# Kernel tuning notes

Measured on AMD Instinct MI355X. Metric: run time of the kernel, lower is better.

## Reference

```python
import jax, jax.numpy as jnp
import numpy as np

N, H, E, K, C, M = 4096, 512, 512, 64, 128, 4  # tokens, hidden, embed, categories, children/cat, max_num_children
IN = E + H  # LSTMCell input size


def setup_inputs() -> dict:
    key = jax.random.key(0)
    ks = jax.random.split(key, 12)
    s = 0.05
    return {
        "et": jax.random.normal(ks[0], (N, H), jnp.float32),
        "x": jax.random.normal(ks[1], (N, IN), jnp.float32),
        "h": jax.random.normal(ks[2], (N, H), jnp.float32),
        "c": jax.random.normal(ks[3], (N, H), jnp.float32),
        "cat": jax.random.randint(ks[4], (N,), 0, K, jnp.int32),
        "ci": jax.random.randint(ks[5], (N,), 0, M, jnp.int32),
        # per-category prediction Linear(hidden_size -> |children(category)|)
        "W_lin": jax.random.normal(ks[6], (K, C, H), jnp.float32) * s,
        "b_lin": jax.random.normal(ks[7], (K, C), jnp.float32) * s,
        # per-child-index LSTMCell(embedding+hidden -> hidden), torch gate order i,f,g,o
        "W_ih": jax.random.normal(ks[8], (M, 4 * H, IN), jnp.float32) * s,
        "W_hh": jax.random.normal(ks[9], (M, 4 * H, H), jnp.float32) * s,
        "b_ih": jax.random.normal(ks[10], (M, 4 * H), jnp.float32) * s,
        "b_hh": jax.random.normal(ks[11], (M, 4 * H), jnp.float32) * s,
    }


def reference(et, x, h, c, cat, ci, W_lin, b_lin, W_ih, W_hh, b_ih, b_hh):
    # get_log_odds: route each token to its category's Linear (gather weights, per-token matvec)
    Wg = W_lin[cat]                                   # [N, C, H]
    log_odds = jnp.einsum('nh,nch->nc', et, Wg) + b_lin[cat]  # [N, C]

    # get_next: LSTMCell selected by child_index. Only M=4 cells, so compute all
    # cells' gates densely (efficient GEMMs) and select with a one-hot mix.
    gates_all = (jnp.einsum('ni,kgi->nkg', x, W_ih)
                 + jnp.einsum('nh,kgh->nkg', h, W_hh)
                 + (b_ih + b_hh)[None])               # [N, M, 4H]
    sel = jax.nn.one_hot(ci, M, dtype=gates_all.dtype)  # [N, M]
    gates = jnp.einsum('nkg,nk->ng', gates_all, sel)     # [N, 4H]
    i_, f_, g_, o_ = jnp.split(gates, 4, axis=-1)
    c2 = jax.nn.sigmoid(f_) * c + jax.nn.sigmoid(i_) * jnp.tanh(g_)
    h2 = jax.nn.sigmoid(o_) * jnp.tanh(c2)
    return log_odds, h2, c2
```

## Files before the change

kernel.cpp:

```cpp
#include <hip/hip_runtime.h>
#include <hip/hip_bf16.h>
#include <stdint.h>

#define NTOK 4096
#define HID  512
#define INSZ 1024
#define KIN  1536
#define KCAT 64
#define CCH  128
#define MCELL 4
#define G4H  2048
#define SLOTS 4608

typedef unsigned short u16;
typedef __bf16 bf16x8 __attribute__((ext_vector_type(8)));
typedef float  f32x4  __attribute__((ext_vector_type(4)));

__device__ __forceinline__ u16 f2bf(float f) {
    unsigned u = __float_as_uint(f);
    u += 0x7fffu + ((u >> 16) & 1u);
    return (u16)(u >> 16);
}
__device__ __forceinline__ float bf2f(u16 v) {
    return __uint_as_float(((unsigned)v) << 16);
}
__device__ __forceinline__ void store_bf8(u16* p, float4 a, float4 b) {
    ushort4 r0, r1;
    r0.x = f2bf(a.x); r0.y = f2bf(a.y); r0.z = f2bf(a.z); r0.w = f2bf(a.w);
    r1.x = f2bf(b.x); r1.y = f2bf(b.y); r1.z = f2bf(b.z); r1.w = f2bf(b.w);
    *reinterpret_cast<ushort4*>(p) = r0;
    *reinterpret_cast<ushort4*>(p + 4) = r1;
}
__device__ __forceinline__ void gl16(const u16* g, u16* l) {
    __builtin_amdgcn_global_load_lds((const __attribute__((address_space(1))) void*)g,
                                     (__attribute__((address_space(3))) void*)l, 16, 0, 0);
}

#define CH_W  (8192 * 192)
#define CH_L  (8192 * 64)
#define CH_A  (4097 * 192)
#define CH_TOT (CH_W + CH_L + CH_A)
#define PK_BLOCKS 2048

__global__ __launch_bounds__(256) void fat_pack(
    const float* __restrict__ x, const float* __restrict__ h,
    const float* __restrict__ Wih, const float* __restrict__ Whh,
    const float* __restrict__ W_lin,
    const int* __restrict__ ci, const int* __restrict__ cat,
    int* __restrict__ meta, int* __restrict__ perm_ci, int* __restrict__ perm_cat,
    u16* __restrict__ A_tok, u16* __restrict__ Wb, u16* __restrict__ Wlin)
{
    if (blockIdx.x == 0) {
        __shared__ int cnt_ci[MCELL], cur_ci[MCELL];
        __shared__ int cnt_cat[KCAT], cur_cat[KCAT];
        int tid = threadIdx.x;
        if (tid < MCELL) cnt_ci[tid] = 0;
        if (tid < KCAT)  cnt_cat[tid] = 0;
        __syncthreads();
        for (int t = tid; t < NTOK; t += 256) {
            atomicAdd(&cnt_ci[ci[t]], 1);
            atomicAdd(&cnt_cat[cat[t]], 1);
        }
        __syncthreads();
        if (tid == 0) {
            int off = 0;
            for (int m = 0; m < MCELL; ++m) {
                int p = (cnt_ci[m] + 127) & ~127;
                meta[m] = p; meta[4 + m] = off; cur_ci[m] = off; off += p;
            }
            off = 0;
            for (int i = 0; i < 128; ++i) meta[136 + i] = -1;
            for (int k = 0; k < KCAT; ++k) {
                int p = (cnt_cat[k] + 63) & ~63;
                meta[8 + k] = p; meta[72 + k] = off; cur_cat[k] = off;
                for (int i = 0; i < p / 64; ++i) meta[136 + off / 64 + i] = k;
                off += p;
            }
        }
        __syncthreads();
        for (int i = tid; i < SLOTS; i += 256) perm_ci[i] = -1;
        for (int i = tid; i < 8192; i += 256) perm_cat[i] = -1;
        __syncthreads();
        for (int t = tid; t < NTOK; t += 256) {
            perm_ci[atomicAdd(&cur_ci[ci[t]], 1)] = t;
            perm_cat[atomicAdd(&cur_cat[cat[t]], 1)] = t;
        }
        return;
    }
    for (int i = (blockIdx.x - 1) * 256 + threadIdx.x; i < CH_TOT; i += (PK_BLOCKS - 1) * 256) {
        if (i < CH_W) {
            int row = i / 192, cc = i - row * 192;
            int m = row >> 11, j = row & 2047;
            int srow = (j & 3) * HID + (j >> 2);
            int c = cc * 8;
            const float* src = (c < INSZ) ? (Wih + ((size_t)m * G4H + srow) * INSZ + c)
                                          : (Whh + ((size_t)m * G4H + srow) * HID + (c - INSZ));
            store_bf8(Wb + (size_t)row * KIN + c,
                      *(const float4*)src, *(const float4*)(src + 4));
        } else if (i < CH_W + CH_L) {
            int i2 = i - CH_W;
            int row = i2 >> 6, cc = i2 & 63;
            const float* src = W_lin + (size_t)row * HID + cc * 8;
            store_bf8(Wlin + (size_t)row * HID + cc * 8,
                      *(const float4*)src, *(const float4*)(src + 4));
        } else {
            int i3 = i - (CH_W + CH_L);
            int row = i3 / 192, cc = i3 - row * 192;
            int c = cc * 8;
            u16* dst = A_tok + (size_t)row * KIN + c;
            if (row == NTOK) {
                *reinterpret_cast<int4*>(dst) = make_int4(0, 0, 0, 0);
            } else {
                const float* src = (c < INSZ) ? (x + (size_t)row * INSZ + c)
                                              : (h + (size_t)row * HID + (c - INSZ));
                store_bf8(dst, *(const float4*)src, *(const float4*)(src + 4));
            }
        }
    }
}

#define FENCE() __builtin_amdgcn_sched_barrier(0)

__global__ __launch_bounds__(256, 2) void mega_gemm(
    const u16* __restrict__ A_tok,
    const u16* __restrict__ Wb,
    const u16* __restrict__ Wlin,
    const float* __restrict__ et,
    const float* __restrict__ b_lin,
    const float* __restrict__ c,
    const float* __restrict__ b_ih,
    const float* __restrict__ b_hh,
    const int* __restrict__ meta,
    const int* __restrict__ perm_ci,
    const int* __restrict__ perm_cat,
    float* __restrict__ out)
{
    __shared__ __align__(16) u16 S[32768];
    __shared__ int sperm[128];

    int tid = threadIdx.x;
    int lane = tid & 63, wave = tid >> 6;
    int qd = lane >> 4, l15 = lane & 15;
    int rsw = l15 & 7;

    int id = blockIdx.x;
    if (id < 2048) {
        int g = id & 63;
        int rt = id >> 6;
        int m = g >> 4, ct = g & 15;
        int pcnt = meta[m];
        if (rt * 128 >= pcnt) return;
        int row0 = meta[4 + m] + rt * 128;

        if (tid < 128) sperm[tid] = perm_ci[row0 + tid];
        __syncthreads();

        const u16* gA[4]; const u16* gB[4];
        int qq[4];
        #pragma unroll
        for (int j = 0; j < 4; ++j) {
            int q = j * 256 + tid;
            int row = q >> 3, kc = (q & 7) ^ (row & 7);
            int t = sperm[row];
            gA[j] = A_tok + (size_t)(t >= 0 ? t : NTOK) * KIN + kc * 8;
            gB[j] = Wb + ((size_t)m * G4H + ct * 128 + row) * KIN + kc * 8;
            qq[j] = q * 8;
        }

        int wm = wave >> 1, wn = wave & 1;

        f32x4 acc[4][4];
        #pragma unroll
        for (int i = 0; i < 4; ++i)
            #pragma unroll
            for (int j = 0; j < 4; ++j)
                acc[i][j] = (f32x4){0.f, 0.f, 0.f, 0.f};

#define STAGE(ABASE, BBASE) do { \
        _Pragma("unroll") \
        for (int j = 0; j < 4; ++j) { gl16(gA[j], &S[(ABASE) + qq[j]]); gA[j] += 64; } \
        _Pragma("unroll") \
        for (int j = 0; j < 4; ++j) { gl16(gB[j], &S[(BBASE) + qq[j]]); gB[j] += 64; } \
    } while (0)

#define GEMM_STEP(ABASE, BBASE) do { \
        _Pragma("unroll") \
        for (int ks2 = 0; ks2 < 2; ++ks2) { \
            int ch = (ks2 * 4 + qd) ^ rsw; \
            bf16x8 fb[4]; \
            _Pragma("unroll") \
            for (int tj = 0; tj < 4; ++tj) \
                fb[tj] = *reinterpret_cast<const bf16x8*>(&S[(BBASE) + (wn * 64 + tj * 16 + l15) * 64 + ch * 8]); \
            _Pragma("unroll") \
            for (int ti = 0; ti < 4; ++ti) { \
                bf16x8 fa = *reinterpret_cast<const bf16x8*>(&S[(ABASE) + (wm * 64 + ti * 16 + l15) * 64 + ch * 8]); \
                _Pragma("unroll") \
                for (int tj = 0; tj < 4; ++tj) \
                    acc[ti][tj] = __builtin_amdgcn_mfma_f32_16x16x32_bf16(fa, fb[tj], acc[ti][tj], 0, 0, 0); \
            } \
        } \
    } while (0)

        STAGE(0, 16384);
        for (int ks = 0; ks < 24; ks += 2) {
            STAGE(8192, 24576);
            asm volatile("s_waitcnt vmcnt(8)" ::: "memory");
            FENCE();
            __builtin_amdgcn_s_barrier();
            FENCE();
            GEMM_STEP(0, 16384);
            FENCE();
            __builtin_amdgcn_s_barrier();
            FENCE();
            if (ks + 2 < 24) {
                STAGE(0, 16384);
                asm volatile("s_waitcnt vmcnt(8)" ::: "memory");
            } else {
                asm volatile("s_waitcnt vmcnt(0)" ::: "memory");
            }
            FENCE();
            __builtin_amdgcn_s_barrier();
            FENCE();
            GEMM_STEP(8192, 24576);
            FENCE();
            __builtin_amdgcn_s_barrier();
            FENCE();
        }
#undef STAGE
#undef GEMM_STEP

        int gt = l15 & 3;
        float bias[4];
        #pragma unroll
        for (int tj = 0; tj < 4; ++tj) {
            int u = ct * 32 + wn * 16 + tj * 4 + (l15 >> 2);
            bias[tj] = b_ih[m * G4H + gt * HID + u] + b_hh[m * G4H + gt * HID + u];
        }
        int b0 = lane & 1, b1 = lane & 2;
        const size_t o_h2 = (size_t)NTOK * CCH;
        const size_t o_c2 = o_h2 + (size_t)NTOK * HID;
        #pragma unroll
        for (int ti = 0; ti < 4; ++ti) {
            int t = sperm[wm * 64 + ti * 16 + qd * 4 + (lane & 3)];
            #pragma unroll
            for (int tj = 0; tj < 4; ++tj) {
                float v0 = acc[ti][tj][0] + bias[tj];
                float v1 = acc[ti][tj][1] + bias[tj];
                float v2 = acc[ti][tj][2] + bias[tj];
                float v3 = acc[ti][tj][3] + bias[tj];
                float tmp;
                tmp = __shfl_xor(b0 ? v0 : v1, 1); if (b0) v0 = tmp; else v1 = tmp;
                tmp = __shfl_xor(b0 ? v2 : v3, 1); if (b0) v2 = tmp; else v3 = tmp;
                tmp = __shfl_xor(b1 ? v0 : v2, 2); if (b1) v0 = tmp; else v2 = tmp;
                tmp = __shfl_xor(b1 ? v1 : v3, 2); if (b1) v1 = tmp; else v3 = tmp;
                if (t >= 0) {
                    int u = ct * 32 + wn * 16 + tj * 4 + (l15 >> 2);
                    float si = 1.f / (1.f + __expf(-v0));
                    float sf = 1.f / (1.f + __expf(-v1));
                    float tg = tanhf(v2);
                    float so = 1.f / (1.f + __expf(-v3));
                    float cold = c[(size_t)t * HID + u];
                    float c2 = sf * cold + si * tg;
                    float h2 = so * tanhf(c2);
                    out[o_h2 + (size_t)t * HID + u] = h2;
                    out[o_c2 + (size_t)t * HID + u] = c2;
                }
            }
        }
    } else {
        u16* As = S;
        u16* Bs = S + 8192;
        int rtl = id - 2048;
        int k = meta[136 + rtl];
        if (k < 0) return;
        int r0 = rtl * 64;

        if (tid < 64) sperm[tid] = perm_cat[r0 + tid];
        __syncthreads();

        int rb = tid >> 3;
        int kc = (tid & 7) ^ (rb & 7);

        const u16* gW[4]; u16* lW[4];
        #pragma unroll
        for (int i = 0; i < 4; ++i) {
            gW[i] = Wlin + ((size_t)k * CCH + i * 32 + rb) * HID + kc * 8;
            lW[i] = As + (i * 256 + wave * 64) * 8;
        }
        int ar = tid >> 2;
        int acp = tid & 3;
        int at = sperm[ar];
        const float* asrc = (at >= 0) ? (et + (size_t)at * HID) : nullptr;

        f32x4 acc[4][2];
        #pragma unroll
        for (int i = 0; i < 4; ++i) {
            acc[i][0] = (f32x4){0.f, 0.f, 0.f, 0.f};
            acc[i][1] = (f32x4){0.f, 0.f, 0.f, 0.f};
        }

        for (int kk = 0; kk < HID; kk += 64) {
            #pragma unroll
            for (int i = 0; i < 4; ++i) { gl16(gW[i], lW[i]); gW[i] += 64; }
            #pragma unroll
            for (int j = 0; j < 2; ++j) {
                int dch = acp * 2 + j;
                int sch = dch ^ (ar & 7);
                u16* dst = &Bs[ar * 64 + dch * 8];
                if (asrc) {
                    const float* s = asrc + kk + sch * 8;
                    store_bf8(dst, *(const float4*)s, *(const float4*)(s + 4));
                } else {
                    *reinterpret_cast<int4*>(dst) = make_int4(0, 0, 0, 0);
                }
            }
            __syncthreads();
            #pragma unroll
            for (int ks2 = 0; ks2 < 2; ++ks2) {
                int ch = (ks2 * 4 + qd) ^ rsw;
                bf16x8 fa[4], fb[2];
                #pragma unroll
                for (int ti = 0; ti < 4; ++ti)
                    fa[ti] = *reinterpret_cast<const bf16x8*>(&Bs[(ti * 16 + l15) * 64 + ch * 8]);
                #pragma unroll
                for (int tj = 0; tj < 2; ++tj)
                    fb[tj] = *reinterpret_cast<const bf16x8*>(&As[(wave * 32 + tj * 16 + l15) * 64 + ch * 8]);
                #pragma unroll
                for (int ti = 0; ti < 4; ++ti)
                    #pragma unroll
                    for (int tj = 0; tj < 2; ++tj)
                        acc[ti][tj] = __builtin_amdgcn_mfma_f32_16x16x32_bf16(fa[ti], fb[tj], acc[ti][tj], 0, 0, 0);
            }
            __syncthreads();
        }

        #pragma unroll
        for (int ti = 0; ti < 4; ++ti) {
            #pragma unroll
            for (int tj = 0; tj < 2; ++tj) {
                int n = wave * 32 + tj * 16 + l15;
                float bias = b_lin[k * CCH + n];
                #pragma unroll
                for (int rr = 0; rr < 4; ++rr) {
                    int row = ti * 16 + qd * 4 + rr;
                    int t = sperm[row];
                    if (t >= 0)
                        out[(size_t)t * CCH + n] = acc[ti][tj][rr] + bias;
                }
            }
        }
    }
}

extern "C" void kernel_launch(void* const* d_in, const int* in_sizes, int n_in,
                              void* d_out, int out_size, void* d_ws, size_t ws_size,
                              hipStream_t stream) {
    const float* et    = (const float*)d_in[0];
    const float* x     = (const float*)d_in[1];
    const float* h     = (const float*)d_in[2];
    const float* c     = (const float*)d_in[3];
    const int*   cat   = (const int*)d_in[4];
    const int*   ci    = (const int*)d_in[5];
    const float* W_lin = (const float*)d_in[6];
    const float* b_lin = (const float*)d_in[7];
    const float* W_ih  = (const float*)d_in[8];
    const float* W_hh  = (const float*)d_in[9];
    const float* b_ih  = (const float*)d_in[10];
    const float* b_hh  = (const float*)d_in[11];
    float* out = (float*)d_out;

    char* ws = (char*)d_ws;
    int* meta     = (int*)ws;
    int* perm_ci  = (int*)(ws + 2048);
    int* perm_cat = (int*)(ws + 22528);
    u16* A_tok    = (u16*)(ws + 55296);
    u16* Wb       = (u16*)(ws + 12641280);
    u16* Wlin     = (u16*)(ws + 37807104);

    fat_pack<<<PK_BLOCKS, 256, 0, stream>>>(x, h, W_ih, W_hh, W_lin, ci, cat,
                                            meta, perm_ci, perm_cat, A_tok, Wb, Wlin);

    mega_gemm<<<2048 + 128, 256, 0, stream>>>(A_tok, Wb, Wlin, et, b_lin, c,
                                              b_ih, b_hh, meta, perm_ci, perm_cat, out);
}
```

Measured before the change: 232.1 us.

## Enlarge LSTM GEMM tiles to 256x256 with 512 threads and triple-buffered K=32 pipeline

The LSTM gate GEMM moves from 128x128 tiles with 256 threads to 256x256 tiles with 512 threads (8 waves, 8x4 MFMA accumulators each). It also switches to a three-slab LDS ring with K=32 stages and raises MFMA wave priority. Per-cell padding grows to 256 rows and the category offsets are computed with a parallel prefix scan instead of a serial loop. The category Linear blocks now pack two 64-row tiles per 512-thread block. The larger tiles aim to cut global/LDS traffic per MFMA, at the cost of more padding waste, higher register pressure and fewer blocks.

```diff
diff --git a/kernel.cpp b/kernel.cpp
--- a/kernel.cpp
+++ b/kernel.cpp
@@ -10,7 +10,7 @@
 #define CCH  128
 #define MCELL 4
 #define G4H  2048
-#define SLOTS 4608
+#define SLOTS 5120
 
 typedef unsigned short u16;
 typedef __bf16 bf16x8 __attribute__((ext_vector_type(8)));
@@ -53,6 +53,7 @@
     if (blockIdx.x == 0) {
         __shared__ int cnt_ci[MCELL], cur_ci[MCELL];
         __shared__ int cnt_cat[KCAT], cur_cat[KCAT];
+        __shared__ int scan_cat[KCAT];
         int tid = threadIdx.x;
         if (tid < MCELL) cnt_ci[tid] = 0;
         if (tid < KCAT)  cnt_cat[tid] = 0;
@@ -62,20 +63,27 @@
             atomicAdd(&cnt_cat[cat[t]], 1);
         }
         __syncthreads();
-        if (tid == 0) {
+        for (int i = tid; i < 128; i += 256) meta[136 + i] = -1;
+        if (tid < MCELL) {
             int off = 0;
-            for (int m = 0; m < MCELL; ++m) {
-                int p = (cnt_ci[m] + 127) & ~127;
-                meta[m] = p; meta[4 + m] = off; cur_ci[m] = off; off += p;
-            }
-            off = 0;
-            for (int i = 0; i < 128; ++i) meta[136 + i] = -1;
-            for (int k = 0; k < KCAT; ++k) {
-                int p = (cnt_cat[k] + 63) & ~63;
-                meta[8 + k] = p; meta[72 + k] = off; cur_cat[k] = off;
-                for (int i = 0; i < p / 64; ++i) meta[136 + off / 64 + i] = k;
-                off += p;
-            }
+            for (int i = 0; i < tid; ++i) off += (cnt_ci[i] + 255) & ~255;
+            int p = (cnt_ci[tid] + 255) & ~255;
+            meta[tid] = p; meta[4 + tid] = off; cur_ci[tid] = off;
+        }
+        if (tid < KCAT) scan_cat[tid] = (cnt_cat[tid] + 63) & ~63;
+        __syncthreads();
+        for (int d = 1; d < KCAT; d <<= 1) {
+            int v = 0;
+            if (tid < KCAT && tid >= d) v = scan_cat[tid - d];
+            __syncthreads();
+            if (tid < KCAT) scan_cat[tid] += v;
+            __syncthreads();
+        }
+        if (tid < KCAT) {
+            int p = (cnt_cat[tid] + 63) & ~63;
+            int off = scan_cat[tid] - p;
+            meta[8 + tid] = p; meta[72 + tid] = off; cur_cat[tid] = off;
+            for (int i = 0; i < p / 64; ++i) meta[136 + off / 64 + i] = tid;
         }
         __syncthreads();
         for (int i = tid; i < SLOTS; i += 256) perm_ci[i] = -1;
@@ -120,8 +128,9 @@
 }
 
 #define FENCE() __builtin_amdgcn_sched_barrier(0)
-
-__global__ __launch_bounds__(256, 2) void mega_gemm(
+#define SLAB 16384
+
+__global__ __launch_bounds__(512, 2) void mega_gemm(
     const u16* __restrict__ A_tok,
     const u16* __restrict__ Wb,
     const u16* __restrict__ Wlin,
@@ -135,113 +144,117 @@
     const int* __restrict__ perm_cat,
     float* __restrict__ out)
 {
-    __shared__ __align__(16) u16 S[32768];
-    __shared__ int sperm[128];
+    __shared__ __align__(16) u16 S[3 * SLAB];
+    __shared__ int sperm[256];
 
     int tid = threadIdx.x;
-    int lane = tid & 63, wave = tid >> 6;
+    int lane = tid & 63;
     int qd = lane >> 4, l15 = lane & 15;
-    int rsw = l15 & 7;
 
     int id = blockIdx.x;
-    if (id < 2048) {
-        int g = id & 63;
-        int rt = id >> 6;
-        int m = g >> 4, ct = g & 15;
+    if (id < 512) {
+        int g = id & 31, rt = id >> 5;
+        int m = g >> 3, ct = g & 7;
         int pcnt = meta[m];
-        if (rt * 128 >= pcnt) return;
-        int row0 = meta[4 + m] + rt * 128;
-
-        if (tid < 128) sperm[tid] = perm_ci[row0 + tid];
-        __syncthreads();
-
-        const u16* gA[4]; const u16* gB[4];
-        int qq[4];
-        #pragma unroll
-        for (int j = 0; j < 4; ++j) {
-            int q = j * 256 + tid;
-            int row = q >> 3, kc = (q & 7) ^ (row & 7);
-            int t = sperm[row];
-            gA[j] = A_tok + (size_t)(t >= 0 ? t : NTOK) * KIN + kc * 8;
-            gB[j] = Wb + ((size_t)m * G4H + ct * 128 + row) * KIN + kc * 8;
-            qq[j] = q * 8;
-        }
-
-        int wm = wave >> 1, wn = wave & 1;
-
-        f32x4 acc[4][4];
-        #pragma unroll
-        for (int i = 0; i < 4; ++i)
+        if (rt * 256 >= pcnt) return;
+        int row0 = meta[4 + m] + rt * 256;
+
+        if (tid < 256) sperm[tid] = perm_ci[row0 + tid];
+        __syncthreads();
+
+        int sl8 = (tid & 3) * 8;
+        int rA0 = tid >> 2, rA1 = 128 + (tid >> 2);
+        int tA0 = sperm[rA0], tA1 = sperm[rA1];
+        const u16* gA0 = A_tok + (size_t)(tA0 >= 0 ? tA0 : NTOK) * KIN + sl8;
+        const u16* gA1 = A_tok + (size_t)(tA1 >= 0 ? tA1 : NTOK) * KIN + sl8;
+        const u16* gB0 = Wb + ((size_t)m * G4H + ct * 256 + (tid >> 2)) * KIN + sl8;
+        const u16* gB1 = Wb + ((size_t)m * G4H + ct * 256 + 128 + (tid >> 2)) * KIN + sl8;
+        int oA0 = tid * 8, oA1 = (512 + tid) * 8;
+        int oB0 = (1024 + tid) * 8, oB1 = (1536 + tid) * 8;
+
+        int wave = tid >> 6;
+        int wm = wave >> 2, wn = wave & 3;
+
+        f32x4 acc[8][4];
+        #pragma unroll
+        for (int i = 0; i < 8; ++i)
             #pragma unroll
             for (int j = 0; j < 4; ++j)
                 acc[i][j] = (f32x4){0.f, 0.f, 0.f, 0.f};
 
-#define STAGE(ABASE, BBASE) do { \
+#define STAGE(SB, KOFF) do { \
+        gl16(gA0 + (KOFF), &S[(SB) + oA0]); \
+        gl16(gA1 + (KOFF), &S[(SB) + oA1]); \
+        gl16(gB0 + (KOFF), &S[(SB) + oB0]); \
+        gl16(gB1 + (KOFF), &S[(SB) + oB1]); \
+    } while (0)
+
+#define COMPUTE(SB) do { \
+        bf16x8 fb[4]; \
         _Pragma("unroll") \
-        for (int j = 0; j < 4; ++j) { gl16(gA[j], &S[(ABASE) + qq[j]]); gA[j] += 64; } \
+        for (int tj = 0; tj < 4; ++tj) \
+            fb[tj] = *reinterpret_cast<const bf16x8*>( \
+                &S[(SB) + (256 + wn * 64 + tj * 16 + l15) * 32 + qd * 8]); \
+        __builtin_amdgcn_s_setprio(1); \
         _Pragma("unroll") \
-        for (int j = 0; j < 4; ++j) { gl16(gB[j], &S[(BBASE) + qq[j]]); gB[j] += 64; } \
-    } while (0)
-
-#define GEMM_STEP(ABASE, BBASE) do { \
-        _Pragma("unroll") \
-        for (int ks2 = 0; ks2 < 2; ++ks2) { \
-            int ch = (ks2 * 4 + qd) ^ rsw; \
-            bf16x8 fb[4]; \
+        for (int ti = 0; ti < 8; ++ti) { \
+            bf16x8 fa = *reinterpret_cast<const bf16x8*>( \
+                &S[(SB) + (wm * 128 + ti * 16 + l15) * 32 + qd * 8]); \
             _Pragma("unroll") \
             for (int tj = 0; tj < 4; ++tj) \
-                fb[tj] = *reinterpret_cast<const bf16x8*>(&S[(BBASE) + (wn * 64 + tj * 16 + l15) * 64 + ch * 8]); \
-            _Pragma("unroll") \
-            for (int ti = 0; ti < 4; ++ti) { \
-                bf16x8 fa = *reinterpret_cast<const bf16x8*>(&S[(ABASE) + (wm * 64 + ti * 16 + l15) * 64 + ch * 8]); \
-                _Pragma("unroll") \
-                for (int tj = 0; tj < 4; ++tj) \
-                    acc[ti][tj] = __builtin_amdgcn_mfma_f32_16x16x32_bf16(fa, fb[tj], acc[ti][tj], 0, 0, 0); \
-            } \
+                acc[ti][tj] = __builtin_amdgcn_mfma_f32_16x16x32_bf16(fa, fb[tj], acc[ti][tj], 0, 0, 0); \
         } \
+        __builtin_amdgcn_s_setprio(0); \
     } while (0)
 
-        STAGE(0, 16384);
-        for (int ks = 0; ks < 24; ks += 2) {
-            STAGE(8192, 24576);
+        STAGE(0, 0);
+        STAGE(SLAB, 32);
+        int koff = 64;
+        int cC = 0, cS = 2;
+        for (int s = 0; s < 46; ++s) {
+            STAGE(cS * SLAB, koff);
+            koff += 32;
             asm volatile("s_waitcnt vmcnt(8)" ::: "memory");
             FENCE();
             __builtin_amdgcn_s_barrier();
             FENCE();
-            GEMM_STEP(0, 16384);
+            COMPUTE(cC * SLAB);
             FENCE();
             __builtin_amdgcn_s_barrier();
             FENCE();
-            if (ks + 2 < 24) {
-                STAGE(0, 16384);
-                asm volatile("s_waitcnt vmcnt(8)" ::: "memory");
-            } else {
-                asm volatile("s_waitcnt vmcnt(0)" ::: "memory");
-            }
-            FENCE();
-            __builtin_amdgcn_s_barrier();
-            FENCE();
-            GEMM_STEP(8192, 24576);
-            FENCE();
-            __builtin_amdgcn_s_barrier();
-            FENCE();
-        }
+            cC = (cC == 2) ? 0 : cC + 1;
+            cS = (cS == 2) ? 0 : cS + 1;
+        }
+        asm volatile("s_waitcnt vmcnt(4)" ::: "memory");
+        FENCE();
+        __builtin_amdgcn_s_barrier();
+        FENCE();
+        COMPUTE(cC * SLAB);
+        cC = (cC == 2) ? 0 : cC + 1;
+        FENCE();
+        __builtin_amdgcn_s_barrier();
+        FENCE();
+        asm volatile("s_waitcnt vmcnt(0)" ::: "memory");
+        FENCE();
+        __builtin_amdgcn_s_barrier();
+        FENCE();
+        COMPUTE(cC * SLAB);
 #undef STAGE
-#undef GEMM_STEP
+#undef COMPUTE
 
         int gt = l15 & 3;
         float bias[4];
         #pragma unroll
         for (int tj = 0; tj < 4; ++tj) {
-            int u = ct * 32 + wn * 16 + tj * 4 + (l15 >> 2);
+            int u = ct * 64 + wn * 16 + tj * 4 + (l15 >> 2);
             bias[tj] = b_ih[m * G4H + gt * HID + u] + b_hh[m * G4H + gt * HID + u];
         }
         int b0 = lane & 1, b1 = lane & 2;
         const size_t o_h2 = (size_t)NTOK * CCH;
         const size_t o_c2 = o_h2 + (size_t)NTOK * HID;
         #pragma unroll
-        for (int ti = 0; ti < 4; ++ti) {
-            int t = sperm[wm * 64 + ti * 16 + qd * 4 + (lane & 3)];
+        for (int ti = 0; ti < 8; ++ti) {
+            int t = sperm[wm * 128 + ti * 16 + qd * 4 + (lane & 3)];
             #pragma unroll
             for (int tj = 0; tj < 4; ++tj) {
                 float v0 = acc[ti][tj][0] + bias[tj];
@@ -254,7 +267,7 @@
                 tmp = __shfl_xor(b1 ? v0 : v2, 2); if (b1) v0 = tmp; else v2 = tmp;
                 tmp = __shfl_xor(b1 ? v1 : v3, 2); if (b1) v1 = tmp; else v3 = tmp;
                 if (t >= 0) {
-                    int u = ct * 32 + wn * 16 + tj * 4 + (l15 >> 2);
+                    int u = ct * 64 + wn * 16 + tj * 4 + (l15 >> 2);
                     float si = 1.f / (1.f + __expf(-v0));
                     float sf = 1.f / (1.f + __expf(-v1));
                     float tg = tanhf(v2);
@@ -268,28 +281,35 @@
             }
         }
     } else {
-        u16* As = S;
-        u16* Bs = S + 8192;
-        int rtl = id - 2048;
+        int half = tid >> 8;
+        int tid2 = tid & 255;
+        int wave2 = tid2 >> 6;
+        int rsw = l15 & 7;
+        u16* As = S + half * 12288;
+        u16* Bs = As + 8192;
+        int* sp = sperm + half * 64;
+
+        int rtl = (id - 512) * 2 + half;
         int k = meta[136 + rtl];
-        if (k < 0) return;
+        int valid = (k >= 0);
+        if (!valid) k = 0;
         int r0 = rtl * 64;
 
-        if (tid < 64) sperm[tid] = perm_cat[r0 + tid];
-        __syncthreads();
-
-        int rb = tid >> 3;
-        int kc = (tid & 7) ^ (rb & 7);
+        if (tid2 < 64) sp[tid2] = valid ? perm_cat[r0 + tid2] : -1;
+        __syncthreads();
+
+        int rb = tid2 >> 3;
+        int kc = (tid2 & 7) ^ (rb & 7);
 
         const u16* gW[4]; u16* lW[4];
         #pragma unroll
         for (int i = 0; i < 4; ++i) {
             gW[i] = Wlin + ((size_t)k * CCH + i * 32 + rb) * HID + kc * 8;
-            lW[i] = As + (i * 256 + wave * 64) * 8;
-        }
-        int ar = tid >> 2;
-        int acp = tid & 3;
-        int at = sperm[ar];
+            lW[i] = As + (i * 256 + wave2 * 64) * 8;
+        }
+        int ar = tid2 >> 2;
+        int acp = tid2 & 3;
+        int at = sp[ar];
         const float* asrc = (at >= 0) ? (et + (size_t)at * HID) : nullptr;
 
         f32x4 acc[4][2];
@@ -324,7 +344,7 @@
                     fa[ti] = *reinterpret_cast<const bf16x8*>(&Bs[(ti * 16 + l15) * 64 + ch * 8]);
                 #pragma unroll
                 for (int tj = 0; tj < 2; ++tj)
-                    fb[tj] = *reinterpret_cast<const bf16x8*>(&As[(wave * 32 + tj * 16 + l15) * 64 + ch * 8]);
+                    fb[tj] = *reinterpret_cast<const bf16x8*>(&As[(wave2 * 32 + tj * 16 + l15) * 64 + ch * 8]);
                 #pragma unroll
                 for (int ti = 0; ti < 4; ++ti)
                     #pragma unroll
@@ -338,12 +358,12 @@
         for (int ti = 0; ti < 4; ++ti) {
             #pragma unroll
             for (int tj = 0; tj < 2; ++tj) {
-                int n = wave * 32 + tj * 16 + l15;
+                int n = wave2 * 32 + tj * 16 + l15;
                 float bias = b_lin[k * CCH + n];
                 #pragma unroll
                 for (int rr = 0; rr < 4; ++rr) {
                     int row = ti * 16 + qd * 4 + rr;
-                    int t = sperm[row];
+                    int t = sp[row];
                     if (t >= 0)
                         out[(size_t)t * CCH + n] = acc[ti][tj][rr] + bias;
                 }
@@ -380,6 +400,6 @@
     fat_pack<<<PK_BLOCKS, 256, 0, stream>>>(x, h, W_ih, W_hh, W_lin, ci, cat,
                                             meta, perm_ci, perm_cat, A_tok, Wb, Wlin);
 
-    mega_gemm<<<2048 + 128, 256, 0, stream>>>(A_tok, Wb, Wlin, et, b_lin, c,
-                                              b_ih, b_hh, meta, perm_ci, perm_cat, out);
-}
+    mega_gemm<<<512 + 64, 512, 0, stream>>>(A_tok, Wb, Wlin, et, b_lin, c,
+                                            b_ih, b_hh, meta, perm_ci, perm_cat, out);
+}
```

New measurement: 244.6 us. 5.4% more time.
